# Kernel optimization log

Hardware: AMD Instinct MI355X
Metric: run time of the kernel (lower is better)

Reference implementation:

```python
import jax, jax.numpy as jnp
import numpy as np

NU, NI = 100000, 50000
N = NU + NI
CU, CI = 100, 100
D = 64
NL = 3
NNZ = 4_000_000
CNNZ = 5000
B = 4096


def setup_inputs() -> dict:
    key = jax.random.key(0)
    ks = jax.random.split(key, 24)
    def edges(k1, k2, k3, nnz, n):
        return (jax.random.randint(k1, (nnz,), 0, n, dtype=jnp.int32),
                jax.random.randint(k2, (nnz,), 0, n, dtype=jnp.int32),
                jax.random.uniform(k3, (nnz,), dtype=jnp.float32) * 0.05)
    ar, ac, av = edges(ks[0], ks[1], ks[2], NNZ, N)
    s1r, s1c, s1v = edges(ks[3], ks[4], ks[5], NNZ, N)
    s2r, s2c, s2v = edges(ks[6], ks[7], ks[8], NNZ, N)
    cr, cc, cv = edges(ks[9], ks[10], ks[11], CNNZ, CU + CI)
    return {
        "user_emb": jax.random.normal(ks[12], (NU, D), dtype=jnp.float32) * 0.1,
        "item_emb": jax.random.normal(ks[13], (NI, D), dtype=jnp.float32) * 0.1,
        "adj_rows": ar, "adj_cols": ac, "adj_vals": av,
        "sg1_rows": s1r, "sg1_cols": s1c, "sg1_vals": s1v,
        "sg2_rows": s2r, "sg2_cols": s2c, "sg2_vals": s2v,
        "uc": jax.random.uniform(ks[14], (NU, CU), dtype=jnp.float32),
        "ic": jax.random.uniform(ks[15], (NI, CI), dtype=jnp.float32),
        "cg_rows": cr, "cg_cols": cc, "cg_vals": cv,
        "users": jax.random.randint(ks[16], (B,), 0, NU, dtype=jnp.int32),
        "items": jax.random.randint(ks[17], (B,), 0, NI, dtype=jnp.int32),
        "neg_items": jax.random.randint(ks[18], (B,), 0, NI, dtype=jnp.int32),
    }


def _gcn(rows, cols, vals, ego, n):
    """n_layers of SpMM propagation + mean over layer outputs (incl. layer 0)."""
    acc = ego
    x = ego
    for _ in range(NL):
        x = jax.ops.segment_sum(vals[:, None] * x[cols], rows, num_segments=n)
        acc = acc + x
    return acc / (NL + 1)


def reference(user_emb, item_emb,
              adj_rows, adj_cols, adj_vals,
              sg1_rows, sg1_cols, sg1_vals,
              sg2_rows, sg2_cols, sg2_vals,
              uc, ic, cg_rows, cg_cols, cg_vals,
              users, items, neg_items):
    ego = jnp.concatenate([user_emb, item_emb], axis=0)  # [N, D]
    e0 = _gcn(adj_rows, adj_cols, adj_vals, ego, N)
    e1 = _gcn(sg1_rows, sg1_cols, sg1_vals, ego, N)
    e2 = _gcn(sg2_rows, sg2_cols, sg2_vals, ego, N)
    # community GCN: project node embeddings onto community space, propagate, lift back
    ucf = uc.T @ user_emb                                # [CU, D]
    icf = ic.T @ item_emb                                # [CI, D]
    ec = _gcn(cg_rows, cg_cols, cg_vals,
              jnp.concatenate([ucf, icf], axis=0), CU + CI)
    u3 = uc @ ec[:CU]                                    # [NU, D]
    i3 = ic @ ec[CU:]                                    # [NI, D]
    user_f = jnp.concatenate([e0[:NU], e1[:NU], e2[:NU], u3], axis=1)  # [NU, 4D]
    item_f = jnp.concatenate([e0[NU:], e1[NU:], e2[NU:], i3], axis=1)  # [NI, 4D]
    ue = user_f[users]
    ie = item_f[items]
    ne = item_f[neg_items]
    # sup_logits = <u, i_pos> - <u, i_neg>
    return jnp.sum(ue * (ie - ne), axis=-1)
```

## Files before the change

### kernel.cpp

```cpp
#include <hip/hip_runtime.h>
#include <hip/hip_fp16.h>
#include <cstdint>
#include <cstddef>

#define NU_ 100000
#define NI_ 50000
#define NN_ 150000
#define D_  64
#define NNZ_ 4000000
#define CN_ 200
#define CNNZ_ 5000
#define B_ 4096

#define NB2   512
#define RPB2  293
#define SLICE 40
#define NBLK  512
#define ECAP  8448

#define PROJB 1024

#define SCALE_ 32.0f
#define INVS_  (1.0f / 32.0f)
#define VSC_   256.0f
#define IVSC_  (1.0f / 256.0f)

typedef float v2f __attribute__((ext_vector_type(2)));

__device__ __forceinline__ float cv8(unsigned char b) {
    return __builtin_amdgcn_cvt_f32_fp8((int)b, 0);
}


__global__ __launch_bounds__(256) void k_tofp8(const float* __restrict__ a,
                                               const float* __restrict__ b,
                                               unsigned char* __restrict__ dst) {
    size_t off = ((size_t)blockIdx.x * 256 + threadIdx.x) * 4;
    if (off >= (size_t)NN_ * D_) return;
    const float* src = (off < (size_t)NU_ * D_) ? a + off : b + (off - (size_t)NU_ * D_);
    float4 f = *(const float4*)src;
    int p = 0;
    p = __builtin_amdgcn_cvt_pk_fp8_f32(f.x * SCALE_, f.y * SCALE_, p, false);
    p = __builtin_amdgcn_cvt_pk_fp8_f32(f.z * SCALE_, f.w * SCALE_, p, true);
    *(unsigned*)(dst + off) = (unsigned)p;
}

__global__ __launch_bounds__(256) void k_bin(const int* __restrict__ rows,
                                             const int* __restrict__ cols,
                                             const float* __restrict__ vals,
                                             int* __restrict__ bcnt,
                                             int2* __restrict__ gbuf) {
    __shared__ int lcur[NB2];
    int t = threadIdx.x;
    for (int i = t; i < NB2; i += 256) lcur[i] = 0;
    __syncthreads();
    size_t blockbase = (size_t)blockIdx.x * NB2 * SLICE;

    for (int base = blockIdx.x * 1024; base < NNZ_; base += gridDim.x * 1024) {
        int i0 = base + t * 4;
        if (i0 < NNZ_) {
            int4   r4 = *(const int4*)(rows + i0);
            int4   c4 = *(const int4*)(cols + i0);
            float4 v4 = *(const float4*)(vals + i0);
            #pragma unroll
            for (int k = 0; k < 4; k++) {
                int r = (k == 0) ? r4.x : (k == 1) ? r4.y : (k == 2) ? r4.z : r4.w;
                int c = (k == 0) ? c4.x : (k == 1) ? c4.y : (k == 2) ? c4.z : c4.w;
                float v = (k == 0) ? v4.x : (k == 1) ? v4.y : (k == 2) ? v4.z : v4.w;
                int b  = r / RPB2;
                int rl = r - b * RPB2;
                int pos = atomicAdd(&lcur[b], 1);
                if (pos < SLICE)
                    gbuf[blockbase + (size_t)b * SLICE + pos] =
                        make_int2((rl << 18) | c, __float_as_int(v));
            }
        }
    }
    __syncthreads();
    for (int i = t; i < NB2; i += 256)
        bcnt[(size_t)blockIdx.x * NB2 + i] = min(lcur[i], SLICE);
}


__global__ void k_btot(const int* __restrict__ bcnt, int* __restrict__ btot) {
    __shared__ int s[256];
    int b = blockIdx.x, t = threadIdx.x;
    int sum = 0;
    for (int sl = t; sl < NBLK; sl += 256) sum += bcnt[(size_t)sl * NB2 + b];
    s[t] = sum;
    __syncthreads();
    for (int o = 128; o > 0; o >>= 1) {
        if (t < o) s[t] += s[t + o];
        __syncthreads();
    }
    if (t == 0) btot[b] = s[0];
}

__global__ void k_bscan(const int* __restrict__ btot, int* __restrict__ bbase,
                        int* __restrict__ row_ptr) {
    __shared__ int s[NB2];
    int t = threadIdx.x;
    int v = btot[t];
    s[t] = v;
    __syncthreads();
    for (int o = 1; o < NB2; o <<= 1) {
        int x = (t >= o) ? s[t - o] : 0;
        __syncthreads();
        s[t] += x;
        __syncthreads();
    }
    bbase[t] = s[t] - v;
    if (t == NB2 - 1) row_ptr[NN_] = s[t];
}


__global__ __launch_bounds__(1024) void k_csr(const int* __restrict__ bcnt,
                                              const int2* __restrict__ gbuf,
                                              const int* __restrict__ bbase,
                                              const int* __restrict__ btot,
                                              int* __restrict__ row_ptr,
                                              unsigned* __restrict__ ep) {
    __shared__ int h[RPB2];
    __shared__ int hx[RPB2];
    __shared__ unsigned estage[ECAP];
    int b = blockIdx.x, t = threadIdx.x;
    for (int i = t; i < RPB2; i += 1024) h[i] = 0;
    __syncthreads();

    int sl = t >> 1, part = t & 1;
    int n = bcnt[(size_t)sl * NB2 + b];
    const int2* src = gbuf + ((size_t)sl * NB2 + b) * SLICE;

    for (int i = part; i < n; i += 2) {
        int rl = ((unsigned)src[i].x) >> 18;
        atomicAdd(&h[rl], 1);
    }
    __syncthreads();

    if (t < RPB2) hx[t] = h[t];
    __syncthreads();
    for (int o = 1; o < RPB2; o <<= 1) {
        int x = 0;
        if (t < RPB2 && t >= o) x = hx[t - o];
        __syncthreads();
        if (t < RPB2) hx[t] += x;
        __syncthreads();
    }

    int base = bbase[b];
    int r0 = b * RPB2;
    if (t < RPB2) {
        int excl = hx[t] - h[t];
        if (r0 + t < NN_) row_ptr[r0 + t] = base + excl;
        h[t] = excl;
    }
    __syncthreads();

    for (int i = part; i < n; i += 2) {
        int2 e = src[i];
        int rl = ((unsigned)e.x) >> 18;
        unsigned c = (unsigned)e.x & 0x3FFFFu;
        float v = __int_as_float(e.y) * VSC_;
        unsigned v8 = (unsigned)__builtin_amdgcn_cvt_pk_fp8_f32(v, 0.f, 0, false) & 0xFFu;
        int pos = atomicAdd(&h[rl], 1);
        if (pos < ECAP) estage[pos] = c | (v8 << 24);
    }
    __syncthreads();

    int total = btot[b];
    if (total > ECAP) total = ECAP;
    for (int i = t; i < total; i += 1024) ep[base + i] = estage[i];
}


__global__ __launch_bounds__(256) void k_spmm(const int* __restrict__ rp,
                                              const unsigned* __restrict__ ep,
                                              const unsigned char* __restrict__ xq,
                                              unsigned char* __restrict__ xn) {
    int w = (blockIdx.x * 256 + threadIdx.x) >> 6;
    if (w >= NN_) return;
    int lane = threadIdx.x & 63;
    int oct = lane >> 3;
    int l8  = lane & 7;
    int j0 = rp[w], j1 = rp[w + 1];
    float a0 = 0.f, a1 = 0.f, a2 = 0.f, a3 = 0.f, a4 = 0.f, a5 = 0.f, a6 = 0.f, a7 = 0.f;
    #pragma unroll 2
    for (int j = j0; j < j1; j += 8) {
        int je = j + oct;
        unsigned e = (je < j1) ? ep[je] : 0u;
        float v = __builtin_amdgcn_cvt_f32_fp8((int)e, 3);
        uint2 raw = *(const uint2*)(xq + (size_t)(e & 0x3FFFFu) * D_ + l8 * 8);
        v2f f01 = __builtin_amdgcn_cvt_pk_f32_fp8((int)raw.x, false);
        v2f f23 = __builtin_amdgcn_cvt_pk_f32_fp8((int)raw.x, true);
        v2f f45 = __builtin_amdgcn_cvt_pk_f32_fp8((int)raw.y, false);
        v2f f67 = __builtin_amdgcn_cvt_pk_f32_fp8((int)raw.y, true);
        a0 += v * f01[0]; a1 += v * f01[1]; a2 += v * f23[0]; a3 += v * f23[1];
        a4 += v * f45[0]; a5 += v * f45[1]; a6 += v * f67[0]; a7 += v * f67[1];
    }
    #pragma unroll
    for (int o = 32; o >= 8; o >>= 1) {
        a0 += __shfl_xor(a0, o, 64); a1 += __shfl_xor(a1, o, 64);
        a2 += __shfl_xor(a2, o, 64); a3 += __shfl_xor(a3, o, 64);
        a4 += __shfl_xor(a4, o, 64); a5 += __shfl_xor(a5, o, 64);
        a6 += __shfl_xor(a6, o, 64); a7 += __shfl_xor(a7, o, 64);
    }
    if (lane < 8) {
        int p0 = 0, p1 = 0;
        p0 = __builtin_amdgcn_cvt_pk_fp8_f32(a0 * IVSC_, a1 * IVSC_, p0, false);
        p0 = __builtin_amdgcn_cvt_pk_fp8_f32(a2 * IVSC_, a3 * IVSC_, p0, true);
        p1 = __builtin_amdgcn_cvt_pk_fp8_f32(a4 * IVSC_, a5 * IVSC_, p1, false);
        p1 = __builtin_amdgcn_cvt_pk_fp8_f32(a6 * IVSC_, a7 * IVSC_, p1, true);
        uint2 o2; o2.x = (unsigned)p0; o2.y = (unsigned)p1;
        *(uint2*)(xn + (size_t)w * D_ + l8 * 8) = o2;
    }
}


__global__ __launch_bounds__(256) void k_spmm_s(const int* __restrict__ rp,
                                                const unsigned* __restrict__ ep,
                                                const unsigned char* __restrict__ xq,
                                                const int* __restrict__ users,
                                                const int* __restrict__ items,
                                                const int* __restrict__ negs,
                                                float* __restrict__ x3s) {
    int s = (blockIdx.x * 256 + threadIdx.x) >> 6;
    if (s >= 3 * B_) return;
    int lane = threadIdx.x & 63;
    int oct = lane >> 3;
    int l8  = lane & 7;
    int node;
    if (s < B_)          node = users[s];
    else if (s < 2 * B_) node = NU_ + items[s - B_];
    else                 node = NU_ + negs[s - 2 * B_];
    int j0 = rp[node], j1 = rp[node + 1];
    float a0 = 0.f, a1 = 0.f, a2 = 0.f, a3 = 0.f, a4 = 0.f, a5 = 0.f, a6 = 0.f, a7 = 0.f;
    #pragma unroll 2
    for (int j = j0; j < j1; j += 8) {
        int je = j + oct;
        unsigned e = (je < j1) ? ep[je] : 0u;
        float v = __builtin_amdgcn_cvt_f32_fp8((int)e, 3);
        uint2 raw = *(const uint2*)(xq + (size_t)(e & 0x3FFFFu) * D_ + l8 * 8);
        v2f f01 = __builtin_amdgcn_cvt_pk_f32_fp8((int)raw.x, false);
        v2f f23 = __builtin_amdgcn_cvt_pk_f32_fp8((int)raw.x, true);
        v2f f45 = __builtin_amdgcn_cvt_pk_f32_fp8((int)raw.y, false);
        v2f f67 = __builtin_amdgcn_cvt_pk_f32_fp8((int)raw.y, true);
        a0 += v * f01[0]; a1 += v * f01[1]; a2 += v * f23[0]; a3 += v * f23[1];
        a4 += v * f45[0]; a5 += v * f45[1]; a6 += v * f67[0]; a7 += v * f67[1];
    }
    #pragma unroll
    for (int o = 32; o >= 8; o >>= 1) {
        a0 += __shfl_xor(a0, o, 64); a1 += __shfl_xor(a1, o, 64);
        a2 += __shfl_xor(a2, o, 64); a3 += __shfl_xor(a3, o, 64);
        a4 += __shfl_xor(a4, o, 64); a5 += __shfl_xor(a5, o, 64);
        a6 += __shfl_xor(a6, o, 64); a7 += __shfl_xor(a7, o, 64);
    }
    if (lane < 8) {
        float* dst = x3s + (size_t)s * D_ + l8 * 8;
        *(float4*)dst       = make_float4(a0 * IVSC_, a1 * IVSC_, a2 * IVSC_, a3 * IVSC_);
        *(float4*)(dst + 4) = make_float4(a4 * IVSC_, a5 * IVSC_, a6 * IVSC_, a7 * IVSC_);
    }
}


template<bool FIRST>
__global__ void k_dot_graph(const float* __restrict__ ue, const float* __restrict__ ie,
                            const unsigned char* __restrict__ x1,
                            const unsigned char* __restrict__ x2,
                            const float* __restrict__ x3s,
                            const int* __restrict__ users, const int* __restrict__ items,
                            const int* __restrict__ negs, float* __restrict__ out) {
    int w = (blockIdx.x * blockDim.x + threadIdx.x) >> 6;
    int lane = threadIdx.x & 63;
    if (w >= B_) return;
    int u = users[w], ip = items[w], in_ = negs[w];
    size_t ou = (size_t)u * D_ + lane;
    size_t oi = (size_t)(NU_ + ip) * D_ + lane;
    size_t on = (size_t)(NU_ + in_) * D_ + lane;
    float du = ue[(size_t)u * D_ + lane]
             + (cv8(x1[ou]) + cv8(x2[ou]) + x3s[(size_t)w * D_ + lane]) * INVS_;
    float di = ie[(size_t)ip * D_ + lane]
             + (cv8(x1[oi]) + cv8(x2[oi]) + x3s[(size_t)(B_ + w) * D_ + lane]) * INVS_;
    float dn = ie[(size_t)in_ * D_ + lane]
             + (cv8(x1[on]) + cv8(x2[on]) + x3s[(size_t)(2 * B_ + w) * D_ + lane]) * INVS_;
    float p = du * (di - dn);
    for (int o = 32; o > 0; o >>= 1) p += __shfl_xor(p, o, 64);
    if (lane == 0) {
        if (FIRST) out[w] = p * 0.0625f;
        else       out[w] += p * 0.0625f;
    }
}


__global__ __launch_bounds__(256) void k_proj(const float* __restrict__ mat,
                                              const float* __restrict__ emb,
                                              int n, float* __restrict__ pbuf) {
    __shared__ float se[8 * 64];
    __shared__ float sc[8 * 100];
    int t = threadIdx.x;
    int d = t & 63, c0 = t >> 6;
    float a[25];
    #pragma unroll
    for (int k = 0; k < 25; k++) a[k] = 0.f;

    int upb = (n + gridDim.x - 1) / gridDim.x;
    int u0 = blockIdx.x * upb;
    int u1 = min(u0 + upb, n);
    int ub = u0;
    for (; ub + 8 <= u1; ub += 8) {
        const float4* e4 = (const float4*)(emb + (size_t)ub * 64);
        const float4* c4 = (const float4*)(mat + (size_t)ub * 100);
        float4* se4 = (float4*)se;
        float4* sc4 = (float4*)sc;
        for (int idx = t; idx < 328; idx += 256) {
            if (idx < 128) se4[idx] = e4[idx];
            else           sc4[idx - 128] = c4[idx - 128];
        }
        __syncthreads();
        #pragma unroll
        for (int ul = 0; ul < 8; ++ul) {
            float ev = se[(ul << 6) + d];
            #pragma unroll
            for (int k = 0; k < 25; k++)
                a[k] += sc[ul * 100 + c0 + (k << 2)] * ev;
        }
        __syncthreads();
    }
    if (ub < u1) {
        int m = u1 - ub;
        for (int idx = t; idx < m * 64; idx += 256) se[idx] = emb[(size_t)ub * 64 + idx];
        for (int idx = t; idx < m * 100; idx += 256) sc[idx] = mat[(size_t)ub * 100 + idx];
        __syncthreads();
        for (int ul = 0; ul < m; ++ul) {
            float ev = se[(ul << 6) + d];
            #pragma unroll
            for (int k = 0; k < 25; k++)
                a[k] += sc[ul * 100 + c0 + (k << 2)] * ev;
        }
    }
    float* dst = pbuf + (size_t)blockIdx.x * 6400;
    #pragma unroll
    for (int k = 0; k < 25; k++)
        dst[t + (k << 8)] = a[k];
}

__global__ __launch_bounds__(256) void k_preduce(const float* __restrict__ pbuf,
                                                 float* __restrict__ dst) {
    int e = blockIdx.x * 256 + threadIdx.x;
    const float* src = pbuf + (size_t)blockIdx.y * 128 * 6400 + e;
    float s = 0.f;
    #pragma unroll 8
    for (int p = 0; p < 128; p++) s += src[(size_t)p * 6400];
    atomicAdd(&dst[e], s);
}


__global__ void k_cspmm(const int* __restrict__ r, const int* __restrict__ c,
                        const float* __restrict__ v, const float* __restrict__ x,
                        float* __restrict__ xn) {
    int w = (blockIdx.x * blockDim.x + threadIdx.x) >> 6;
    int lane = threadIdx.x & 63;
    if (w >= CNNZ_) return;
    int rr = r[w], cc = c[w];
    float vv = v[w];
    atomicAdd(&xn[rr * 64 + lane], vv * x[cc * 64 + lane]);
}

__global__ void k_cesum(const float* __restrict__ cego, const float* __restrict__ cb1,
                        const float* __restrict__ cb2, const float* __restrict__ cb3,
                        float* __restrict__ cacc) {
    int i = blockIdx.x * blockDim.x + threadIdx.x;
    if (i < CN_ * D_) cacc[i] = cego[i] + cb1[i] + cb2[i] + cb3[i];
}


__global__ void k_dot_comm(const float* __restrict__ uc, const float* __restrict__ ic,
                           const float* __restrict__ cacc, const int* __restrict__ users,
                           const int* __restrict__ items, const int* __restrict__ negs,
                           float* __restrict__ out) {
    int w = (blockIdx.x * blockDim.x + threadIdx.x) >> 6;
    int lane = threadIdx.x & 63;
    if (w >= B_) return;
    int u = users[w], ip = items[w], in_ = negs[w];
    float u3 = 0.f, i3p = 0.f, i3n = 0.f;
    for (int cc = 0; cc < 100; ++cc) {
        float evU = cacc[cc * 64 + lane];
        float evI = cacc[(100 + cc) * 64 + lane];
        u3  += uc[(size_t)u * 100 + cc] * evU;
        i3p += ic[(size_t)ip * 100 + cc] * evI;
        i3n += ic[(size_t)in_ * 100 + cc] * evI;
    }
    float p = u3 * (i3p - i3n);
    for (int o = 32; o > 0; o >>= 1) p += __shfl_xor(p, o, 64);
    if (lane == 0) out[w] += p * 0.0625f;
}


static inline char* alignp(char*& p, size_t bytes) {
    char* r = p;
    p += (bytes + 255) & ~(size_t)255;
    return r;
}

extern "C" void kernel_launch(void* const* d_in, const int* in_sizes, int n_in,
                              void* d_out, int out_size, void* d_ws, size_t ws_size,
                              hipStream_t stream) {
    const float* uemb = (const float*)d_in[0];
    const float* iemb = (const float*)d_in[1];
    const float* uc   = (const float*)d_in[11];
    const float* ic   = (const float*)d_in[12];
    const int*   cgr  = (const int*)d_in[13];
    const int*   cgc  = (const int*)d_in[14];
    const float* cgv  = (const float*)d_in[15];
    const int*   users = (const int*)d_in[16];
    const int*   items = (const int*)d_in[17];
    const int*   negs  = (const int*)d_in[18];
    float* out = (float*)d_out;

    char* p = (char*)d_ws;
    char*  A      = alignp(p, (size_t)NBLK * NB2 * SLICE * 8);
    unsigned char* egoq = (unsigned char*)alignp(p, (size_t)NN_ * D_);
    unsigned* ep  = (unsigned*)alignp(p, (size_t)NNZ_ * 4);
    float* x3s    = (float*)alignp(p, (size_t)3 * B_ * D_ * 4);
    int*   row_ptr= (int*)  alignp(p, (size_t)(NN_ + 1) * 4);
    int*   bcnt   = (int*)  alignp(p, (size_t)NBLK * NB2 * 4);
    int*   btot   = (int*)  alignp(p, NB2 * 4);
    int*   bbase  = (int*)  alignp(p, NB2 * 4);
    float* cego   = (float*)alignp(p, (size_t)CN_ * D_ * 4);
    float* cb1    = (float*)alignp(p, (size_t)CN_ * D_ * 4);
    float* cb2    = (float*)alignp(p, (size_t)CN_ * D_ * 4);
    float* cb3    = (float*)alignp(p, (size_t)CN_ * D_ * 4);
    float* cacc   = (float*)alignp(p, (size_t)CN_ * D_ * 4);

    int2*          gbuf = (int2*)A;
    unsigned char* xq1  = (unsigned char*)A;
    unsigned char* xq2  = (unsigned char*)(A + (size_t)NN_ * D_);
    float*         pbuf = (float*)A;

    const int gSp = (NN_ * 64) / 256;
    const int gS3 = (3 * B_ * 64) / 256;
    const int gB  = (B_ * 64) / 256;
    const int gC  = (CNNZ_ * 64) / 256;
    const int gCE = (CN_ * D_ + 255) / 256;
    const int gTQ = (NN_ * D_ / 4 + 255) / 256;

    k_tofp8<<<gTQ, 256, 0, stream>>>(uemb, iemb, egoq);

    for (int g = 0; g < 3; ++g) {
        const int*   rows = (const int*)d_in[2 + g * 3];
        const int*   cols = (const int*)d_in[3 + g * 3];
        const float* vals = (const float*)d_in[4 + g * 3];

        k_bin  <<<NBLK, 256, 0, stream>>>(rows, cols, vals, bcnt, gbuf);
        k_btot <<<NB2, 256, 0, stream>>>(bcnt, btot);
        k_bscan<<<1, NB2, 0, stream>>>(btot, bbase, row_ptr);
        k_csr  <<<NB2, 1024, 0, stream>>>(bcnt, gbuf, bbase, btot, row_ptr, ep);

        k_spmm<<<gSp, 256, 0, stream>>>(row_ptr, ep, egoq, xq1);
        k_spmm<<<gSp, 256, 0, stream>>>(row_ptr, ep, xq1, xq2);
        k_spmm_s<<<gS3, 256, 0, stream>>>(row_ptr, ep, xq2, users, items, negs, x3s);

        if (g == 0)
            k_dot_graph<true ><<<gB, 256, 0, stream>>>(uemb, iemb, xq1, xq2, x3s,
                                                       users, items, negs, out);
        else
            k_dot_graph<false><<<gB, 256, 0, stream>>>(uemb, iemb, xq1, xq2, x3s,
                                                       users, items, negs, out);
    }

    hipMemsetAsync(cego, 0, (size_t)CN_ * D_ * 4, stream);
    k_proj<<<PROJB, 256, 0, stream>>>(uc, uemb, NU_, pbuf);
    k_preduce<<<dim3(25, 8), 256, 0, stream>>>(pbuf, cego);
    k_proj<<<PROJB, 256, 0, stream>>>(ic, iemb, NI_, pbuf);
    k_preduce<<<dim3(25, 8), 256, 0, stream>>>(pbuf, cego + 100 * 64);

    hipMemsetAsync(cb1, 0, (size_t)CN_ * D_ * 4, stream);
    k_cspmm<<<gC, 256, 0, stream>>>(cgr, cgc, cgv, cego, cb1);
    hipMemsetAsync(cb2, 0, (size_t)CN_ * D_ * 4, stream);
    k_cspmm<<<gC, 256, 0, stream>>>(cgr, cgc, cgv, cb1, cb2);
    hipMemsetAsync(cb3, 0, (size_t)CN_ * D_ * 4, stream);
    k_cspmm<<<gC, 256, 0, stream>>>(cgr, cgc, cgv, cb2, cb3);
    k_cesum<<<gCE, 256, 0, stream>>>(cego, cb1, cb2, cb3, cacc);

    k_dot_comm<<<gB, 256, 0, stream>>>(uc, ic, cacc, users, items, negs, out);
}
```

Baseline: 921.5 us.

## Single-pass CSR staging, nontemporal loads, deeper unroll, fused community sum

The CSR build kernel now reads each binned edge from global memory once. It compacts edges into shared memory with a wave-ballot counter and keeps the row ids beside them, then scatters to final positions, instead of reading gbuf twice. Edge and COO streams use nontemporal loads, and the SpMM inner loop unroll rises from 2 to 4. The community-layer memsets are merged into one, and the cesum kernel is folded into k_dot_comm. Scattering straight to global memory gives less coalesced writes and uses more shared memory.

```diff
diff --git a/kernel.cpp b/kernel.cpp
--- a/kernel.cpp
+++ b/kernel.cpp
@@ -26,6 +26,8 @@
 #define IVSC_  (1.0f / 256.0f)
 
 typedef float v2f __attribute__((ext_vector_type(2)));
+typedef int   v4i __attribute__((ext_vector_type(4)));
+typedef float v4f __attribute__((ext_vector_type(4)));
 
 __device__ __forceinline__ float cv8(unsigned char b) {
     return __builtin_amdgcn_cvt_f32_fp8((int)b, 0);
@@ -45,6 +47,7 @@
     *(unsigned*)(dst + off) = (unsigned)p;
 }
 
+
 __global__ __launch_bounds__(256) void k_bin(const int* __restrict__ rows,
                                              const int* __restrict__ cols,
                                              const float* __restrict__ vals,
@@ -59,9 +62,9 @@
     for (int base = blockIdx.x * 1024; base < NNZ_; base += gridDim.x * 1024) {
         int i0 = base + t * 4;
         if (i0 < NNZ_) {
-            int4   r4 = *(const int4*)(rows + i0);
-            int4   c4 = *(const int4*)(cols + i0);
-            float4 v4 = *(const float4*)(vals + i0);
+            v4i r4 = __builtin_nontemporal_load((const v4i*)(rows + i0));
+            v4i c4 = __builtin_nontemporal_load((const v4i*)(cols + i0));
+            v4f v4 = __builtin_nontemporal_load((const v4f*)(vals + i0));
             #pragma unroll
             for (int k = 0; k < 4; k++) {
                 int r = (k == 0) ? r4.x : (k == 1) ? r4.y : (k == 2) ? r4.z : r4.w;
@@ -117,23 +120,46 @@
 __global__ __launch_bounds__(1024) void k_csr(const int* __restrict__ bcnt,
                                               const int2* __restrict__ gbuf,
                                               const int* __restrict__ bbase,
-                                              const int* __restrict__ btot,
                                               int* __restrict__ row_ptr,
                                               unsigned* __restrict__ ep) {
     __shared__ int h[RPB2];
     __shared__ int hx[RPB2];
-    __shared__ unsigned estage[ECAP];
+    __shared__ unsigned epack[ECAP];
+    __shared__ unsigned short erow[ECAP];
+    __shared__ int ecnt;
     int b = blockIdx.x, t = threadIdx.x;
     for (int i = t; i < RPB2; i += 1024) h[i] = 0;
+    if (t == 0) ecnt = 0;
     __syncthreads();
 
     int sl = t >> 1, part = t & 1;
     int n = bcnt[(size_t)sl * NB2 + b];
     const int2* src = gbuf + ((size_t)sl * NB2 + b) * SLICE;
-
-    for (int i = part; i < n; i += 2) {
-        int rl = ((unsigned)src[i].x) >> 18;
-        atomicAdd(&h[rl], 1);
+    int lane = t & 63;
+
+    for (int i = part; i < SLICE; i += 2) {
+        bool has = (i < n);
+        unsigned long long q = 0;
+        if (has) q = __builtin_nontemporal_load((const unsigned long long*)(src + i));
+        unsigned long long mask = __ballot(has);
+        if (has) {
+            int cnt = __popcll(mask);
+            int pre = __popcll(mask & ((1ULL << lane) - 1ULL));
+            int leader = __ffsll((unsigned long long)mask) - 1;
+            int bs;
+            if (lane == leader) bs = atomicAdd(&ecnt, cnt);
+            bs = __shfl(bs, leader, 64);
+            int si = bs + pre;
+            if (si < ECAP) {
+                unsigned ex = (unsigned)q;
+                int rl = ex >> 18;
+                float v = __int_as_float((int)(q >> 32)) * VSC_;
+                unsigned v8 = (unsigned)__builtin_amdgcn_cvt_pk_fp8_f32(v, 0.f, 0, false) & 0xFFu;
+                epack[si] = (ex & 0x3FFFFu) | (v8 << 24);
+                erow[si] = (unsigned short)rl;
+                atomicAdd(&h[rl], 1);
+            }
+        }
     }
     __syncthreads();
 
@@ -156,20 +182,13 @@
     }
     __syncthreads();
 
-    for (int i = part; i < n; i += 2) {
-        int2 e = src[i];
-        int rl = ((unsigned)e.x) >> 18;
-        unsigned c = (unsigned)e.x & 0x3FFFFu;
-        float v = __int_as_float(e.y) * VSC_;
-        unsigned v8 = (unsigned)__builtin_amdgcn_cvt_pk_fp8_f32(v, 0.f, 0, false) & 0xFFu;
-        int pos = atomicAdd(&h[rl], 1);
-        if (pos < ECAP) estage[pos] = c | (v8 << 24);
-    }
-    __syncthreads();
-
-    int total = btot[b];
+    int total = ecnt;
     if (total > ECAP) total = ECAP;
-    for (int i = t; i < total; i += 1024) ep[base + i] = estage[i];
+    for (int i = t; i < total; i += 1024) {
+        int rl = erow[i];
+        int pos = base + atomicAdd(&h[rl], 1);
+        ep[pos] = epack[i];
+    }
 }
 
 
@@ -184,10 +203,10 @@
     int l8  = lane & 7;
     int j0 = rp[w], j1 = rp[w + 1];
     float a0 = 0.f, a1 = 0.f, a2 = 0.f, a3 = 0.f, a4 = 0.f, a5 = 0.f, a6 = 0.f, a7 = 0.f;
-    #pragma unroll 2
+    #pragma unroll 4
     for (int j = j0; j < j1; j += 8) {
         int je = j + oct;
-        unsigned e = (je < j1) ? ep[je] : 0u;
+        unsigned e = (je < j1) ? __builtin_nontemporal_load(ep + je) : 0u;
         float v = __builtin_amdgcn_cvt_f32_fp8((int)e, 3);
         uint2 raw = *(const uint2*)(xq + (size_t)(e & 0x3FFFFu) * D_ + l8 * 8);
         v2f f01 = __builtin_amdgcn_cvt_pk_f32_fp8((int)raw.x, false);
@@ -234,10 +253,10 @@
     else                 node = NU_ + negs[s - 2 * B_];
     int j0 = rp[node], j1 = rp[node + 1];
     float a0 = 0.f, a1 = 0.f, a2 = 0.f, a3 = 0.f, a4 = 0.f, a5 = 0.f, a6 = 0.f, a7 = 0.f;
-    #pragma unroll 2
+    #pragma unroll 4
     for (int j = j0; j < j1; j += 8) {
         int je = j + oct;
-        unsigned e = (je < j1) ? ep[je] : 0u;
+        unsigned e = (je < j1) ? __builtin_nontemporal_load(ep + je) : 0u;
         float v = __builtin_amdgcn_cvt_f32_fp8((int)e, 3);
         uint2 raw = *(const uint2*)(xq + (size_t)(e & 0x3FFFFu) * D_ + l8 * 8);
         v2f f01 = __builtin_amdgcn_cvt_pk_f32_fp8((int)raw.x, false);
@@ -365,26 +384,21 @@
     atomicAdd(&xn[rr * 64 + lane], vv * x[cc * 64 + lane]);
 }
 
-__global__ void k_cesum(const float* __restrict__ cego, const float* __restrict__ cb1,
-                        const float* __restrict__ cb2, const float* __restrict__ cb3,
-                        float* __restrict__ cacc) {
-    int i = blockIdx.x * blockDim.x + threadIdx.x;
-    if (i < CN_ * D_) cacc[i] = cego[i] + cb1[i] + cb2[i] + cb3[i];
-}
-
 
 __global__ void k_dot_comm(const float* __restrict__ uc, const float* __restrict__ ic,
-                           const float* __restrict__ cacc, const int* __restrict__ users,
-                           const int* __restrict__ items, const int* __restrict__ negs,
-                           float* __restrict__ out) {
+                           const float* __restrict__ cego, const float* __restrict__ cb1,
+                           const float* __restrict__ cb2, const float* __restrict__ cb3,
+                           const int* __restrict__ users, const int* __restrict__ items,
+                           const int* __restrict__ negs, float* __restrict__ out) {
     int w = (blockIdx.x * blockDim.x + threadIdx.x) >> 6;
     int lane = threadIdx.x & 63;
     if (w >= B_) return;
     int u = users[w], ip = items[w], in_ = negs[w];
     float u3 = 0.f, i3p = 0.f, i3n = 0.f;
     for (int cc = 0; cc < 100; ++cc) {
-        float evU = cacc[cc * 64 + lane];
-        float evI = cacc[(100 + cc) * 64 + lane];
+        int eu = cc * 64 + lane, ei = (100 + cc) * 64 + lane;
+        float evU = cego[eu] + cb1[eu] + cb2[eu] + cb3[eu];
+        float evI = cego[ei] + cb1[ei] + cb2[ei] + cb3[ei];
         u3  += uc[(size_t)u * 100 + cc] * evU;
         i3p += ic[(size_t)ip * 100 + cc] * evI;
         i3n += ic[(size_t)in_ * 100 + cc] * evI;
@@ -426,10 +440,8 @@
     int*   btot   = (int*)  alignp(p, NB2 * 4);
     int*   bbase  = (int*)  alignp(p, NB2 * 4);
     float* cego   = (float*)alignp(p, (size_t)CN_ * D_ * 4);
-    float* cb1    = (float*)alignp(p, (size_t)CN_ * D_ * 4);
-    float* cb2    = (float*)alignp(p, (size_t)CN_ * D_ * 4);
-    float* cb3    = (float*)alignp(p, (size_t)CN_ * D_ * 4);
-    float* cacc   = (float*)alignp(p, (size_t)CN_ * D_ * 4);
+    float* cbs    = (float*)alignp(p, (size_t)3 * CN_ * D_ * 4);
+    float* cb1 = cbs, *cb2 = cbs + CN_ * D_, *cb3 = cbs + 2 * CN_ * D_;
 
     int2*          gbuf = (int2*)A;
     unsigned char* xq1  = (unsigned char*)A;
@@ -440,7 +452,6 @@
     const int gS3 = (3 * B_ * 64) / 256;
     const int gB  = (B_ * 64) / 256;
     const int gC  = (CNNZ_ * 64) / 256;
-    const int gCE = (CN_ * D_ + 255) / 256;
     const int gTQ = (NN_ * D_ / 4 + 255) / 256;
 
     k_tofp8<<<gTQ, 256, 0, stream>>>(uemb, iemb, egoq);
@@ -453,7 +464,7 @@
         k_bin  <<<NBLK, 256, 0, stream>>>(rows, cols, vals, bcnt, gbuf);
         k_btot <<<NB2, 256, 0, stream>>>(bcnt, btot);
         k_bscan<<<1, NB2, 0, stream>>>(btot, bbase, row_ptr);
-        k_csr  <<<NB2, 1024, 0, stream>>>(bcnt, gbuf, bbase, btot, row_ptr, ep);
+        k_csr  <<<NB2, 1024, 0, stream>>>(bcnt, gbuf, bbase, row_ptr, ep);
 
         k_spmm<<<gSp, 256, 0, stream>>>(row_ptr, ep, egoq, xq1);
         k_spmm<<<gSp, 256, 0, stream>>>(row_ptr, ep, xq1, xq2);
@@ -473,13 +484,11 @@
     k_proj<<<PROJB, 256, 0, stream>>>(ic, iemb, NI_, pbuf);
     k_preduce<<<dim3(25, 8), 256, 0, stream>>>(pbuf, cego + 100 * 64);
 
-    hipMemsetAsync(cb1, 0, (size_t)CN_ * D_ * 4, stream);
+    hipMemsetAsync(cbs, 0, (size_t)3 * CN_ * D_ * 4, stream);
     k_cspmm<<<gC, 256, 0, stream>>>(cgr, cgc, cgv, cego, cb1);
-    hipMemsetAsync(cb2, 0, (size_t)CN_ * D_ * 4, stream);
     k_cspmm<<<gC, 256, 0, stream>>>(cgr, cgc, cgv, cb1, cb2);
-    hipMemsetAsync(cb3, 0, (size_t)CN_ * D_ * 4, stream);
     k_cspmm<<<gC, 256, 0, stream>>>(cgr, cgc, cgv, cb2, cb3);
-    k_cesum<<<gCE, 256, 0, stream>>>(cego, cb1, cb2, cb3, cacc);
-
-    k_dot_comm<<<gB, 256, 0, stream>>>(uc, ic, cacc, users, items, negs, out);
-}
+
+    k_dot_comm<<<gB, 256, 0, stream>>>(uc, ic, cego, cb1, cb2, cb3,
+                                       users, items, negs, out);
+}
```

Result: slower. 0.9996 ms (+8.5%).
